# Kernel tuning notes

Measured on AMD Instinct MI355X. Metric: run time of the kernel, lower is better.

The kernel has to match this reference:

```python
import jax, jax.numpy as jnp
import numpy as np
from jax import lax

SIGMA, GAMMA, N_ORI = 6.0, 0.5, 6
WAVELENGTHS = (8.0, 10.0, 12.0)
KS = 37  # int(6*sigma)=36 -> +1 to make odd


def make_gabor_kernels():
    # Replicates cv2.getGaborKernel(psi=0); kernel is symmetric under 180-deg
    # rotation so cv2's index flip is a no-op and conv == correlation.
    half = KS // 2
    yy, xx = np.meshgrid(np.arange(-half, half + 1, dtype=np.float64),
                         np.arange(-half, half + 1, dtype=np.float64), indexing='ij')
    ks = []
    for lam in WAVELENGTHS:
        for t in range(N_ORI):
            th = t * np.pi / N_ORI
            xr = xx * np.cos(th) + yy * np.sin(th)
            yr = -xx * np.sin(th) + yy * np.cos(th)
            k = np.exp(-(xr ** 2 + (GAMMA ** 2) * yr ** 2) / (2.0 * SIGMA ** 2)) \
                * np.cos(2.0 * np.pi / lam * xr)
            ks.append(k.astype(np.float32))
    return jnp.asarray(np.stack(ks))[:, None]  # (F=18, 1, 37, 37)


def setup_inputs() -> dict:
    key = jax.random.key(0)
    x = jax.random.normal(key, (8, 3, 256, 256), dtype=jnp.float32)
    return {"x": x, "gabor_kernels": make_gabor_kernels()}


def haar_dwt2(x):
    # Single-level pywt haar dwt2; for even H,W symmetric padding never fires,
    # so each output pixel comes from a disjoint 2x2 block [[a,b],[c,d]].
    B, C, H, W = x.shape
    xb = x.reshape(B, C, H // 2, 2, W // 2, 2)
    a, b = xb[:, :, :, 0, :, 0], xb[:, :, :, 0, :, 1]
    c, d = xb[:, :, :, 1, :, 0], xb[:, :, :, 1, :, 1]
    LL = (a + b + c + d) * 0.5
    LH = (a + b - c - d) * 0.5  # pywt cH ('da'): high along rows
    HL = (a - b + c - d) * 0.5  # pywt cV ('ad'): high along cols
    HH = (a - b - c + d) * 0.5  # pywt cD ('dd')
    sub = jnp.stack([LL, LH, HL, HH], axis=2)  # (B, C, 4, H/2, W/2)
    return sub.reshape(B, C * 4, H // 2, W // 2)


def gabor_bank(x, kernels):
    # One grouped conv replaces the Python C x F conv2d loop. Group-major output
    # channel order (channel outer, filter inner) matches the torch loop order.
    B, C, H, W = x.shape
    F = kernels.shape[0]
    w = jnp.tile(kernels, (C, 1, 1, 1))  # (C*F, 1, KS, KS)
    pad = KS // 2
    return lax.conv_general_dilated(
        x, w, window_strides=(1, 1), padding=[(pad, pad), (pad, pad)],
        dimension_numbers=('NCHW', 'OIHW', 'NCHW'), feature_group_count=C)


def fft_channels(x):
    B, C, H, W = x.shape
    xc = jnp.fft.rfft2(x, norm='ortho')       # (B, C, H, W//2+1)
    mag = jnp.abs(xc)
    ph = jnp.arctan2(xc.imag, xc.real)        # torch.angle
    pad = W - mag.shape[-1]
    pads = [(0, 0), (0, 0), (0, 0), (0, pad)]
    return jnp.concatenate([jnp.pad(mag, pads), jnp.pad(ph, pads)], axis=1)


def reference(x, gabor_kernels):
    dwt = haar_dwt2(x)                 # (B, C*4, H/2, W/2)
    gab = gabor_bank(x, gabor_kernels)  # (B, C*18, H, W)
    fft = fft_channels(x)              # (B, C*2, H, W)
    return (dwt, gab, fft)
```

## Files before the change

### kernel.cpp

```cpp
#include <hip/hip_runtime.h>
#include <math.h>

#define BB 8
#define CC 3
#define HH 256
#define WW 256
#define KSZ 37
#define PD 18

#define DWT_OFF 0
#define GAB_OFF (8*12*128*128)
#define FFT_OFF (GAB_OFF + 8*54*256*256)

#define PSTRIDE 88

#define PREP_BLOCKS 888
#define FFTROW_BLOCKS 768
#define GAB_BLOCKS 1536
#define FFTCOL_BLOCKS 387

typedef short bf16x8 __attribute__((ext_vector_type(8)));
typedef float f32x16 __attribute__((ext_vector_type(16)));

__device__ __forceinline__ unsigned f2bf(float f) {
  unsigned u = __float_as_uint(f);
  return (u + 0x7fffu + ((u >> 16) & 1u)) >> 16;
}

__global__ __launch_bounds__(512) void fused_pre_kernel(
    const float* __restrict__ x, const float* __restrict__ wk,
    ushort* __restrict__ wshc, float* __restrict__ out) {
  __shared__ __align__(16) float smem[4352];
  const int g = blockIdx.x;
  const int tid = threadIdx.x;

  if (g < PREP_BLOCKS) {
    int idx = g * 512 + tid;
    int j = idx & 7; int rest = idx >> 3;
    int l = rest & 63; rest >>= 6;
    int t = rest % 3; rest /= 3;
    int ky = rest % 37; int s = rest / 37;
    int m = l & 31, hi = l >> 5;
    int kk = 16 * t + 8 * hi + j - s;
    float v = 0.0f;
    if (m < 18 && kk >= 0 && kk < 37) v = wk[(m * 37 + ky) * 37 + kk];
    wshc[idx] = (ushort)f2bf(v);
    return;
  }

  const int w = tid >> 6;
  const int t = tid & 63;
  const int rowid = (g - PREP_BLOCKS) * 8 + w;
  float* re  = smem + w * 256;
  float* im  = smem + 2048 + w * 256;
  float* twr = smem + 4096;
  float* twi = smem + 4224;

#pragma unroll
  for (int q = 0; q < 2; ++q) {
    int k = t + q * 64;
    float sn, cs;
    sincosf(-2.0f * (float)M_PI * (float)k / 256.0f, &sn, &cs);
    twr[k] = cs; twi[k] = sn;
  }
  const float* xr = x + (size_t)rowid * 256;
#pragma unroll
  for (int q = 0; q < 4; ++q) {
    int i = t + q * 64;
    int br = __brev((unsigned)i) >> 24;
    re[br] = xr[i];
    im[br] = 0.0f;
  }
  for (int s = 1; s <= 8; ++s) {
    int half = 1 << (s - 1);
    int sh = 8 - s;
#pragma unroll
    for (int q = 0; q < 2; ++q) {
      int j = t + q * 64;
      int gg = j >> (s - 1);
      int p = j & (half - 1);
      int i1 = (gg << s) + p;
      int i2 = i1 + half;
      float cs = twr[p << sh], sn = twi[p << sh];
      float r2 = re[i2], m2 = im[i2];
      float tr = r2 * cs - m2 * sn;
      float ti = r2 * sn + m2 * cs;
      float r1 = re[i1], m1 = im[i1];
      re[i2] = r1 - tr; im[i2] = m1 - ti;
      re[i1] = r1 + tr; im[i1] = m1 + ti;
    }
  }
  const int bc = rowid >> 8;
  const int y  = rowid & 255;
  const int b  = bc / 3, c = bc - b * 3;
  float* magrow = out + FFT_OFF + (size_t)(b * 6 + c) * (HH * WW) + (size_t)y * WW;
  float* phrow  = magrow + (size_t)3 * (HH * WW);
#pragma unroll
  for (int q = 0; q < 2; ++q) {
    int k = t + q * 64;
    magrow[k] = re[k];
    phrow[k]  = im[k];
  }
  if (t == 0) { magrow[128] = re[128]; phrow[128] = im[128]; }
  magrow[129 + t] = 0.0f;
  phrow[129 + t]  = 0.0f;
  if (t < 63) {
    magrow[193 + t] = 0.0f;
    phrow[193 + t]  = 0.0f;
  }
}

#define LOAD_B_SET \
    r0 = *reinterpret_cast<const bf16x8*>(bp); \
    r1 = *reinterpret_cast<const bf16x8*>(bp + 8); \
    r2 = *reinterpret_cast<const bf16x8*>(bp + 16); \
    r3 = *reinterpret_cast<const bf16x8*>(bp + 24); \
    r4 = *reinterpret_cast<const bf16x8*>(bp + 32); \
    r5 = *reinterpret_cast<const bf16x8*>(bp + 40); \
    r6 = *reinterpret_cast<const bf16x8*>(bp + 48); \
    r7 = *reinterpret_cast<const bf16x8*>(bp + 56);
#define MFMA_GROUP(A0, A1, A2) \
    acc0 = __builtin_amdgcn_mfma_f32_32x32x16_bf16(A0, r0, acc0, 0, 0, 0); \
    acc1 = __builtin_amdgcn_mfma_f32_32x32x16_bf16(A0, r1, acc1, 0, 0, 0); \
    acc2 = __builtin_amdgcn_mfma_f32_32x32x16_bf16(A0, r2, acc2, 0, 0, 0); \
    acc3 = __builtin_amdgcn_mfma_f32_32x32x16_bf16(A0, r3, acc3, 0, 0, 0); \
    acc0 = __builtin_amdgcn_mfma_f32_32x32x16_bf16(A1, r2, acc0, 0, 0, 0); \
    acc1 = __builtin_amdgcn_mfma_f32_32x32x16_bf16(A1, r3, acc1, 0, 0, 0); \
    acc2 = __builtin_amdgcn_mfma_f32_32x32x16_bf16(A1, r4, acc2, 0, 0, 0); \
    acc3 = __builtin_amdgcn_mfma_f32_32x32x16_bf16(A1, r5, acc3, 0, 0, 0); \
    acc0 = __builtin_amdgcn_mfma_f32_32x32x16_bf16(A2, r4, acc0, 0, 0, 0); \
    acc1 = __builtin_amdgcn_mfma_f32_32x32x16_bf16(A2, r5, acc1, 0, 0, 0); \
    acc2 = __builtin_amdgcn_mfma_f32_32x32x16_bf16(A2, r6, acc2, 0, 0, 0); \
    acc3 = __builtin_amdgcn_mfma_f32_32x32x16_bf16(A2, r7, acc3, 0, 0, 0);

__global__ __launch_bounds__(512, 4) void fused_main_kernel(
    const float* __restrict__ x, const ushort* __restrict__ wshc,
    float* __restrict__ out) {
  __shared__ __align__(16) float smem[7216];
  const int g = blockIdx.x;
  const int tid = threadIdx.x;

  if (g < GAB_BLOCKS) {
    unsigned* patchU = reinterpret_cast<unsigned*>(smem);
    float* cbuf = smem + 2992;
    const int tile = g & 63;
    const int rest = g >> 6;
    const int cin = rest % 3, b = rest / 3;
    const int tileX = (tile & 7) * 32;
    const int tileY = (tile >> 3) * 32;
    const float* xp = x + (size_t)(b * CC + cin) * (HH * WW);

    for (int idx = tid; idx < 68 * (PSTRIDE / 2); idx += 512) {
      int r = idx / (PSTRIDE / 2), dc = idx - r * (PSTRIDE / 2);
      int gy = tileY + r - PD;
      int gx0 = tileX + 2 * dc - PD;
      float v0 = 0.0f, v1 = 0.0f;
      if ((unsigned)gy < 256u) {
        if ((unsigned)gx0 < 256u)       v0 = xp[gy * WW + gx0];
        if ((unsigned)(gx0 + 1) < 256u) v1 = xp[gy * WW + gx0 + 1];
      }
      patchU[idx] = f2bf(v0) | (f2bf(v1) << 16);
    }
    __syncthreads();

    const int w  = tid >> 6;
    const int l  = tid & 63;
    const int n  = l & 31;
    const int hi = l >> 5;

    f32x16 acc0 = {0.f,0.f,0.f,0.f,0.f,0.f,0.f,0.f,0.f,0.f,0.f,0.f,0.f,0.f,0.f,0.f};
    f32x16 acc1 = acc0, acc2 = acc0, acc3 = acc0;

    const ushort* patchS = reinterpret_cast<const ushort*>(patchU);
    const ushort* ap = wshc + (size_t)w * (37 * 3 * 512) + (size_t)l * 8;
    const ushort* bp = patchS + (size_t)n * PSTRIDE + hi * 8;

    bf16x8 aA0, aA1, aA2, aB0, aB1, aB2;
    bf16x8 r0, r1, r2, r3, r4, r5, r6, r7;

    aA0 = *reinterpret_cast<const bf16x8*>(ap);
    aA1 = *reinterpret_cast<const bf16x8*>(ap + 512);
    aA2 = *reinterpret_cast<const bf16x8*>(ap + 1024);

    for (int kp = 0; kp < 18; ++kp) {
      aB0 = *reinterpret_cast<const bf16x8*>(ap + 1536);
      aB1 = *reinterpret_cast<const bf16x8*>(ap + 2048);
      aB2 = *reinterpret_cast<const bf16x8*>(ap + 2560);
      LOAD_B_SET
      MFMA_GROUP(aA0, aA1, aA2)
      bp += PSTRIDE;
      aA0 = *reinterpret_cast<const bf16x8*>(ap + 3072);
      aA1 = *reinterpret_cast<const bf16x8*>(ap + 3584);
      aA2 = *reinterpret_cast<const bf16x8*>(ap + 4096);
      LOAD_B_SET
      MFMA_GROUP(aB0, aB1, aB2)
      ap += 3072;
      bp += PSTRIDE;
    }
    {
      LOAD_B_SET
      MFMA_GROUP(aA0, aA1, aA2)
    }
    __syncthreads();

    float* outb = out + GAB_OFF + (size_t)(b * 54 + cin * 18) * (HH * WW);
#pragma unroll
    for (int gq = 0; gq < 5; ++gq) {
      if (hi == (gq & 1)) {
        const int rq = gq >> 1;
#pragma unroll
        for (int q = 0; q < 4; ++q) {
          const int e = 4 * rq + q;
          float* crow = &cbuf[(q * 32 + n) * 33 + w];
          crow[0]  = acc0[e];
          crow[8]  = acc1[e];
          crow[16] = acc2[e];
          crow[24] = acc3[e];
        }
      }
      __syncthreads();
#pragma unroll
      for (int it = 0; it < 8; ++it) {
        int idx = tid + it * 512;
        int xo = idx & 31, yo = (idx >> 5) & 31, q = idx >> 10;
        int f = 4 * gq + q;
        if (f < 18)
          outb[(size_t)f * (HH * WW) + (size_t)(tileY + yo) * WW + tileX + xo] =
              cbuf[(q * 32 + yo) * 33 + xo];
      }
      __syncthreads();
    }
    return;
  }

  const int w = tid >> 6;
  const int t = tid & 63;
  const int colid = (g - GAB_BLOCKS) * 8 + w;
  const int bc = colid / 129;
  const int k  = colid - bc * 129;
  const int b  = bc / 3, c = bc - b * 3;
  float* re  = smem + w * 256;
  float* im  = smem + 2048 + w * 256;
  float* twr = smem + 4096;
  float* twi = smem + 4224;

#pragma unroll
  for (int q = 0; q < 2; ++q) {
    int kk = t + q * 64;
    float sn, cs;
    sincosf(-2.0f * (float)M_PI * (float)kk / 256.0f, &sn, &cs);
    twr[kk] = cs; twi[kk] = sn;
  }

  float* magp = out + FFT_OFF + (size_t)(b * 6 + c) * (HH * WW);
  float* php  = magp + (size_t)3 * (HH * WW);
#pragma unroll
  for (int q = 0; q < 4; ++q) {
    int y = t + q * 64;
    int br = __brev((unsigned)y) >> 24;
    re[br] = magp[(size_t)y * WW + k];
    im[br] = php[(size_t)y * WW + k];
  }

  for (int s = 1; s <= 8; ++s) {
    int half = 1 << (s - 1);
    int sh = 8 - s;
#pragma unroll
    for (int q = 0; q < 2; ++q) {
      int j = t + q * 64;
      int gg = j >> (s - 1);
      int p = j & (half - 1);
      int i1 = (gg << s) + p;
      int i2 = i1 + half;
      float cs = twr[p << sh], sn = twi[p << sh];
      float r2 = re[i2], m2 = im[i2];
      float tr = r2 * cs - m2 * sn;
      float ti = r2 * sn + m2 * cs;
      float r1 = re[i1], m1 = im[i1];
      re[i2] = r1 - tr; im[i2] = m1 - ti;
      re[i1] = r1 + tr; im[i1] = m1 + ti;
    }
  }

  const float scale = 1.0f / 256.0f;
#pragma unroll
  for (int q = 0; q < 4; ++q) {
    int u = t + q * 64;
    float r = re[u], m = im[u];
    magp[(size_t)u * WW + k] = sqrtf(r * r + m * m) * scale;
    php[(size_t)u * WW + k]  = atan2f(m, r);
  }
}

__global__ __launch_bounds__(256) void haar_dwt_kernel(
    const float* __restrict__ x, float* __restrict__ out) {
  int idx = blockIdx.x * 256 + threadIdx.x;
  if (idx >= BB * CC * 128 * 128) return;
  int j  = idx & 127;
  int i  = (idx >> 7) & 127;
  int bc = idx >> 14;
  const float* xp = x + (size_t)bc * (HH * WW);
  float2 top = *reinterpret_cast<const float2*>(&xp[(2 * i) * WW + 2 * j]);
  float2 bot = *reinterpret_cast<const float2*>(&xp[(2 * i + 1) * WW + 2 * j]);
  float a = top.x, b = top.y, c = bot.x, d = bot.y;
  int bI = bc / 3, cI = bc % 3;
  float* op = out + DWT_OFF + ((size_t)(bI * 12 + cI * 4) * 128 + i) * 128 + j;
  op[0]     = (a + b + c + d) * 0.5f;
  op[16384] = (a + b - c - d) * 0.5f;
  op[32768] = (a - b + c - d) * 0.5f;
  op[49152] = (a - b - c + d) * 0.5f;
}

extern "C" void kernel_launch(void* const* d_in, const int* in_sizes, int n_in,
                              void* d_out, int out_size, void* d_ws, size_t ws_size,
                              hipStream_t stream) {
  const float* x  = (const float*)d_in[0];
  const float* wk = (const float*)d_in[1];
  float* out = (float*)d_out;

  ushort* wshc = (ushort*)(out + DWT_OFF);

  fused_pre_kernel<<<dim3(PREP_BLOCKS + FFTROW_BLOCKS), dim3(512), 0, stream>>>(
      x, wk, wshc, out);
  fused_main_kernel<<<dim3(GAB_BLOCKS + FFTCOL_BLOCKS), dim3(512), 0, stream>>>(
      x, wshc, out);
  haar_dwt_kernel<<<dim3(1536), dim3(256), 0, stream>>>(x, out);
}
```

Baseline: 167.8 us.

## Split Gabor tile across two 256-thread blocks and double-buffer B fragments

Each Gabor tile is now handled by two 4-wave blocks, each covering half the filter slices, instead of one 8-wave block, so the grid doubles and the FFT column blocks shrink to 4 waves each. The MFMA loop now double-buffers both A and B register sets, prefetching the next row's B fragments from LDS while the current group computes, rather than reloading B right before use. This trades duplicated patch staging (each half reloads the full input patch) and more register pressure for better latency hiding and finer scheduling granularity.

After: 422.8 us. 2.52x slower.

```diff
diff --git a/kernel.cpp b/kernel.cpp
--- a/kernel.cpp
+++ b/kernel.cpp
@@ -16,8 +16,8 @@
 
 #define PREP_BLOCKS 888
 #define FFTROW_BLOCKS 768
-#define GAB_BLOCKS 1536
-#define FFTCOL_BLOCKS 387
+#define GAB_BLOCKS 3072
+#define FFTCOL_BLOCKS 774
 
 typedef short bf16x8 __attribute__((ext_vector_type(8)));
 typedef float f32x16 __attribute__((ext_vector_type(16)));
@@ -110,30 +110,34 @@
   }
 }
 
-#define LOAD_B_SET \
-    r0 = *reinterpret_cast<const bf16x8*>(bp); \
-    r1 = *reinterpret_cast<const bf16x8*>(bp + 8); \
-    r2 = *reinterpret_cast<const bf16x8*>(bp + 16); \
-    r3 = *reinterpret_cast<const bf16x8*>(bp + 24); \
-    r4 = *reinterpret_cast<const bf16x8*>(bp + 32); \
-    r5 = *reinterpret_cast<const bf16x8*>(bp + 40); \
-    r6 = *reinterpret_cast<const bf16x8*>(bp + 48); \
-    r7 = *reinterpret_cast<const bf16x8*>(bp + 56);
-#define MFMA_GROUP(A0, A1, A2) \
-    acc0 = __builtin_amdgcn_mfma_f32_32x32x16_bf16(A0, r0, acc0, 0, 0, 0); \
-    acc1 = __builtin_amdgcn_mfma_f32_32x32x16_bf16(A0, r1, acc1, 0, 0, 0); \
-    acc2 = __builtin_amdgcn_mfma_f32_32x32x16_bf16(A0, r2, acc2, 0, 0, 0); \
-    acc3 = __builtin_amdgcn_mfma_f32_32x32x16_bf16(A0, r3, acc3, 0, 0, 0); \
-    acc0 = __builtin_amdgcn_mfma_f32_32x32x16_bf16(A1, r2, acc0, 0, 0, 0); \
-    acc1 = __builtin_amdgcn_mfma_f32_32x32x16_bf16(A1, r3, acc1, 0, 0, 0); \
-    acc2 = __builtin_amdgcn_mfma_f32_32x32x16_bf16(A1, r4, acc2, 0, 0, 0); \
-    acc3 = __builtin_amdgcn_mfma_f32_32x32x16_bf16(A1, r5, acc3, 0, 0, 0); \
-    acc0 = __builtin_amdgcn_mfma_f32_32x32x16_bf16(A2, r4, acc0, 0, 0, 0); \
-    acc1 = __builtin_amdgcn_mfma_f32_32x32x16_bf16(A2, r5, acc1, 0, 0, 0); \
-    acc2 = __builtin_amdgcn_mfma_f32_32x32x16_bf16(A2, r6, acc2, 0, 0, 0); \
-    acc3 = __builtin_amdgcn_mfma_f32_32x32x16_bf16(A2, r7, acc3, 0, 0, 0);
-
-__global__ __launch_bounds__(512, 4) void fused_main_kernel(
+#define LOAD_B(S, P) \
+    r##S##0 = *reinterpret_cast<const bf16x8*>(P); \
+    r##S##1 = *reinterpret_cast<const bf16x8*>((P) + 8); \
+    r##S##2 = *reinterpret_cast<const bf16x8*>((P) + 16); \
+    r##S##3 = *reinterpret_cast<const bf16x8*>((P) + 24); \
+    r##S##4 = *reinterpret_cast<const bf16x8*>((P) + 32); \
+    r##S##5 = *reinterpret_cast<const bf16x8*>((P) + 40); \
+    r##S##6 = *reinterpret_cast<const bf16x8*>((P) + 48); \
+    r##S##7 = *reinterpret_cast<const bf16x8*>((P) + 56);
+#define LOAD_A(S, P) \
+    a##S##0 = *reinterpret_cast<const bf16x8*>(P); \
+    a##S##1 = *reinterpret_cast<const bf16x8*>((P) + 512); \
+    a##S##2 = *reinterpret_cast<const bf16x8*>((P) + 1024);
+#define MFMA_GROUP(S) \
+    acc0 = __builtin_amdgcn_mfma_f32_32x32x16_bf16(a##S##0, r##S##0, acc0, 0, 0, 0); \
+    acc1 = __builtin_amdgcn_mfma_f32_32x32x16_bf16(a##S##0, r##S##1, acc1, 0, 0, 0); \
+    acc2 = __builtin_amdgcn_mfma_f32_32x32x16_bf16(a##S##0, r##S##2, acc2, 0, 0, 0); \
+    acc3 = __builtin_amdgcn_mfma_f32_32x32x16_bf16(a##S##0, r##S##3, acc3, 0, 0, 0); \
+    acc0 = __builtin_amdgcn_mfma_f32_32x32x16_bf16(a##S##1, r##S##2, acc0, 0, 0, 0); \
+    acc1 = __builtin_amdgcn_mfma_f32_32x32x16_bf16(a##S##1, r##S##3, acc1, 0, 0, 0); \
+    acc2 = __builtin_amdgcn_mfma_f32_32x32x16_bf16(a##S##1, r##S##4, acc2, 0, 0, 0); \
+    acc3 = __builtin_amdgcn_mfma_f32_32x32x16_bf16(a##S##1, r##S##5, acc3, 0, 0, 0); \
+    acc0 = __builtin_amdgcn_mfma_f32_32x32x16_bf16(a##S##2, r##S##4, acc0, 0, 0, 0); \
+    acc1 = __builtin_amdgcn_mfma_f32_32x32x16_bf16(a##S##2, r##S##5, acc1, 0, 0, 0); \
+    acc2 = __builtin_amdgcn_mfma_f32_32x32x16_bf16(a##S##2, r##S##6, acc2, 0, 0, 0); \
+    acc3 = __builtin_amdgcn_mfma_f32_32x32x16_bf16(a##S##2, r##S##7, acc3, 0, 0, 0);
+
+__global__ __launch_bounds__(256, 3) void fused_main_kernel(
     const float* __restrict__ x, const ushort* __restrict__ wshc,
     float* __restrict__ out) {
   __shared__ __align__(16) float smem[7216];
@@ -143,14 +147,15 @@
   if (g < GAB_BLOCKS) {
     unsigned* patchU = reinterpret_cast<unsigned*>(smem);
     float* cbuf = smem + 2992;
-    const int tile = g & 63;
-    const int rest = g >> 6;
-    const int cin = rest % 3, b = rest / 3;
+    const int half = g & 1;
+    const int tile = (g >> 1) & 63;
+    const int img  = g >> 7;
+    const int cin = img % 3, b = img / 3;
     const int tileX = (tile & 7) * 32;
     const int tileY = (tile >> 3) * 32;
     const float* xp = x + (size_t)(b * CC + cin) * (HH * WW);
 
-    for (int idx = tid; idx < 68 * (PSTRIDE / 2); idx += 512) {
+    for (int idx = tid; idx < 68 * (PSTRIDE / 2); idx += 256) {
       int r = idx / (PSTRIDE / 2), dc = idx - r * (PSTRIDE / 2);
       int gy = tileY + r - PD;
       int gx0 = tileX + 2 * dc - PD;
@@ -164,6 +169,7 @@
     __syncthreads();
 
     const int w  = tid >> 6;
+    const int s  = 4 * half + w;
     const int l  = tid & 63;
     const int n  = l & 31;
     const int hi = l >> 5;
@@ -172,35 +178,26 @@
     f32x16 acc1 = acc0, acc2 = acc0, acc3 = acc0;
 
     const ushort* patchS = reinterpret_cast<const ushort*>(patchU);
-    const ushort* ap = wshc + (size_t)w * (37 * 3 * 512) + (size_t)l * 8;
+    const ushort* ap = wshc + (size_t)s * (37 * 3 * 512) + (size_t)l * 8;
     const ushort* bp = patchS + (size_t)n * PSTRIDE + hi * 8;
 
     bf16x8 aA0, aA1, aA2, aB0, aB1, aB2;
-    bf16x8 r0, r1, r2, r3, r4, r5, r6, r7;
-
-    aA0 = *reinterpret_cast<const bf16x8*>(ap);
-    aA1 = *reinterpret_cast<const bf16x8*>(ap + 512);
-    aA2 = *reinterpret_cast<const bf16x8*>(ap + 1024);
-
+    bf16x8 rA0, rA1, rA2, rA3, rA4, rA5, rA6, rA7;
+    bf16x8 rB0, rB1, rB2, rB3, rB4, rB5, rB6, rB7;
+
+    LOAD_A(A, ap)
+    LOAD_B(A, bp)
     for (int kp = 0; kp < 18; ++kp) {
-      aB0 = *reinterpret_cast<const bf16x8*>(ap + 1536);
-      aB1 = *reinterpret_cast<const bf16x8*>(ap + 2048);
-      aB2 = *reinterpret_cast<const bf16x8*>(ap + 2560);
-      LOAD_B_SET
-      MFMA_GROUP(aA0, aA1, aA2)
-      bp += PSTRIDE;
-      aA0 = *reinterpret_cast<const bf16x8*>(ap + 3072);
-      aA1 = *reinterpret_cast<const bf16x8*>(ap + 3584);
-      aA2 = *reinterpret_cast<const bf16x8*>(ap + 4096);
-      LOAD_B_SET
-      MFMA_GROUP(aB0, aB1, aB2)
+      LOAD_A(B, ap + 1536)
+      LOAD_B(B, bp + PSTRIDE)
+      MFMA_GROUP(A)
+      LOAD_A(A, ap + 3072)
+      LOAD_B(A, bp + 2 * PSTRIDE)
+      MFMA_GROUP(B)
       ap += 3072;
-      bp += PSTRIDE;
-    }
-    {
-      LOAD_B_SET
-      MFMA_GROUP(aA0, aA1, aA2)
-    }
+      bp += 2 * PSTRIDE;
+    }
+    MFMA_GROUP(A)
     __syncthreads();
 
     float* outb = out + GAB_OFF + (size_t)(b * 54 + cin * 18) * (HH * WW);
@@ -211,7 +208,7 @@
 #pragma unroll
         for (int q = 0; q < 4; ++q) {
           const int e = 4 * rq + q;
-          float* crow = &cbuf[(q * 32 + n) * 33 + w];
+          float* crow = &cbuf[(q * 32 + n) * 33 + s];
           crow[0]  = acc0[e];
           crow[8]  = acc1[e];
           crow[16] = acc2[e];
@@ -221,12 +218,13 @@
       __syncthreads();
 #pragma unroll
       for (int it = 0; it < 8; ++it) {
-        int idx = tid + it * 512;
-        int xo = idx & 31, yo = (idx >> 5) & 31, q = idx >> 10;
-        int f = 4 * gq + q;
+        int idx = tid + it * 256;
+        int xs = idx & 15, yo = (idx >> 4) & 31, fq = idx >> 9;
+        int xo = (xs >> 2) * 8 + (xs & 3) + 4 * half;
+        int f = 4 * gq + fq;
         if (f < 18)
           outb[(size_t)f * (HH * WW) + (size_t)(tileY + yo) * WW + tileX + xo] =
-              cbuf[(q * 32 + yo) * 33 + xo];
+              cbuf[(fq * 32 + yo) * 33 + xo];
       }
       __syncthreads();
     }
@@ -235,14 +233,14 @@
 
   const int w = tid >> 6;
   const int t = tid & 63;
-  const int colid = (g - GAB_BLOCKS) * 8 + w;
+  const int colid = (g - GAB_BLOCKS) * 4 + w;
   const int bc = colid / 129;
   const int k  = colid - bc * 129;
   const int b  = bc / 3, c = bc - b * 3;
-  float* re  = smem + w * 256;
-  float* im  = smem + 2048 + w * 256;
-  float* twr = smem + 4096;
-  float* twi = smem + 4224;
+  float* re  = smem + w * 512;
+  float* im  = smem + w * 512 + 256;
+  float* twr = smem + 2048;
+  float* twi = smem + 2176;
 
 #pragma unroll
   for (int q = 0; q < 2; ++q) {
@@ -322,7 +320,7 @@
 
   fused_pre_kernel<<<dim3(PREP_BLOCKS + FFTROW_BLOCKS), dim3(512), 0, stream>>>(
       x, wk, wshc, out);
-  fused_main_kernel<<<dim3(GAB_BLOCKS + FFTCOL_BLOCKS), dim3(512), 0, stream>>>(
+  fused_main_kernel<<<dim3(GAB_BLOCKS + FFTCOL_BLOCKS), dim3(256), 0, stream>>>(
       x, wshc, out);
   haar_dwt_kernel<<<dim3(1536), dim3(256), 0, stream>>>(x, out);
 }
```
